# Performance work log

Measured on AMD Instinct MI355X. Metric: run time of the kernel, lower is better.

The kernel has to match this reference:

```python
import jax, jax.numpy as jnp
import numpy as np

# Dimensions
T = 1024      # tokens
D = 1024      # d_model
DFF = 1024    # expert intermediate dim
R = 64        # tucker rank (r_in == r_out)
G = 8         # n_group
E = 32        # experts_per_group
NEXP = G * E  # 256 routed experts
K = 8         # top-k


def setup_inputs() -> dict:
    key = jax.random.key(0)
    ks = jax.random.split(key, 12)
    s = 0.02
    return {
        "x": jax.random.normal(ks[0], (T, D), jnp.float32),
        "Wg": jax.random.normal(ks[1], (D, NEXP), jnp.float32) * s,
        "uin_gate": jax.random.normal(ks[2], (G, D, R), jnp.float32) * s,
        "core_gate": jax.random.normal(ks[3], (G, E, R, R), jnp.float32) * s,
        "uout_gate": jax.random.normal(ks[4], (G, R, DFF), jnp.float32) * s,
        "uin_up": jax.random.normal(ks[5], (G, D, R), jnp.float32) * s,
        "core_up": jax.random.normal(ks[6], (G, E, R, R), jnp.float32) * s,
        "uout_up": jax.random.normal(ks[7], (G, R, DFF), jnp.float32) * s,
        "uin_down": jax.random.normal(ks[8], (G, DFF, R), jnp.float32) * s,
        "core_down": jax.random.normal(ks[9], (G, E, R, R), jnp.float32) * s,
        "uout_down": jax.random.normal(ks[10], (G, R, D), jnp.float32) * s,
    }


def _moe_forward(x, Wg, uin_gate, core_gate, uout_gate,
                 uin_up, core_up, uout_up,
                 uin_down, core_down, uout_down):
    Tn, d = x.shape
    # Router: top-k over 256 experts, softmax over the k logits (fp32 as in torch)
    logits = x @ Wg                                   # [T, NEXP]
    w, sel = jax.lax.top_k(logits, K)                 # [T, K]
    w = jax.nn.softmax(w.astype(jnp.float32), axis=-1).astype(x.dtype)

    e = sel.reshape(-1)                               # [F] global expert id
    g = e // E                                        # [F] group id
    tok = jnp.repeat(jnp.arange(Tn), K)               # [F] source token id
    mask = (g[:, None] == jnp.arange(G)[None, :]).astype(x.dtype)  # [F, G]

    def gather_in(uin):
        # project tokens with every group's u_in once, then gather per pair
        pre = jnp.einsum('td,gdr->gtr', x, uin)       # [G, T, R]
        return pre[g, tok]                            # [F, R]

    def core_apply(xin, core):
        # per-pair Tucker core slice bmm: x.unsqueeze(1) @ core[rel_idx]
        slices = core.reshape(G * E, R, R)[e]         # [F, R, R] gather
        return jnp.einsum('fr,fro->fo', xin, slices)  # [F, R]

    def group_out(h, U):
        # per-pair group-specific projection: h[f] @ U[g_f]
        out = jnp.zeros((h.shape[0], U.shape[-1]), h.dtype)
        for gi in range(G):  # fixed small loop over 8 groups
            out = out + (h * mask[:, gi:gi + 1]) @ U[gi]
        return out

    gate_h = group_out(core_apply(gather_in(uin_gate), core_gate), uout_gate)  # [F, DFF]
    up_h = group_out(core_apply(gather_in(uin_up), core_up), uout_up)          # [F, DFF]
    act = jax.nn.silu(gate_h) * up_h                                           # SwiGLU
    xin_d = group_out(act, uin_down)                                           # [F, R]
    out_f = group_out(core_apply(xin_d, core_down), uout_down)                 # [F, D]
    out_f = out_f * w.reshape(-1)[:, None]
    # scatter-add expert outputs back to tokens
    return jax.ops.segment_sum(out_f, tok, num_segments=Tn)


def reference(x, Wg, uin_gate, core_gate, uout_gate,
              uin_up, core_up, uout_up,
              uin_down, core_down, uout_down):
    return _moe_forward(x, Wg, uin_gate, core_gate, uout_gate,
                        uin_up, core_up, uout_up,
                        uin_down, core_down, uout_down)
```

## Files before the change

### kernel.cpp

```cpp
#include <hip/hip_runtime.h>
#include <hip/hip_bf16.h>
#include <math.h>


#define T_ 1024
#define D_ 1024
#define DFF_ 1024
#define R_ 64
#define G_ 8
#define E_ 32
#define NEXP_ 256
#define K_ 8
#define F_ 8192
#define LKZ_ 8
#define LTB_ 8
#define PKZ_ 2
#define DKZ_ 4
#define LP_ 72

typedef short bf16x8 __attribute__((ext_vector_type(8)));
typedef float f32x4 __attribute__((ext_vector_type(4)));

__device__ __forceinline__ unsigned short f2bf(float f) {
  unsigned int u = __float_as_uint(f);
  u += 0x7fffu + ((u >> 16) & 1u);
  return (unsigned short)(u >> 16);
}

__device__ __forceinline__ void stage_tile(short* dst, const unsigned short* src,
                                           int gp, int tid) {
  for (int idx = tid; idx < 512; idx += 256) {
    int r = idx >> 3, c8 = (idx & 7) << 3;
    *(uint4*)&dst[r * LP_ + c8] = *(const uint4*)&src[(size_t)r * gp + c8];
  }
}

__device__ __forceinline__ void stage_tile_guard(short* dst, const unsigned short* src,
                                                 int gp, int rows_valid, int tid) {
  for (int idx = tid; idx < 512; idx += 256) {
    int r = idx >> 3, c8 = (idx & 7) << 3;
    uint4 v = make_uint4(0u, 0u, 0u, 0u);
    if (r < rows_valid) v = *(const uint4*)&src[(size_t)r * gp + c8];
    *(uint4*)&dst[r * LP_ + c8] = v;
  }
}

__device__ __forceinline__ void mma_strip(const short* As, const short* Bs,
                                          int ms, int lane, f32x4* acc) {
  int lm = lane & 15;
  int lk = (lane >> 4) << 3;
#pragma unroll
  for (int kc = 0; kc < 64; kc += 32) {
    bf16x8 a = *(const bf16x8*)&As[(ms + lm) * LP_ + kc + lk];
#pragma unroll
    for (int nt = 0; nt < 4; ++nt) {
      bf16x8 b = *(const bf16x8*)&Bs[(nt * 16 + lm) * LP_ + kc + lk];
      acc[nt] = __builtin_amdgcn_mfma_f32_16x16x32_bf16(a, b, acc[nt], 0, 0, 0);
    }
  }
}

__global__ __launch_bounds__(256) void k_prep_logits(
    const float* __restrict__ x, const float* __restrict__ Wg,
    const float* __restrict__ s0, const float* __restrict__ s1,
    const float* __restrict__ s2, const float* __restrict__ s3,
    const float* __restrict__ s4, const float* __restrict__ s5,
    unsigned short* __restrict__ xb,
    unsigned short* __restrict__ d0, unsigned short* __restrict__ d1,
    unsigned short* __restrict__ d2, unsigned short* __restrict__ d3,
    unsigned short* __restrict__ d4, unsigned short* __restrict__ d5,
    int* __restrict__ cnt, float* __restrict__ lp) {
  __shared__ float shbuf[64 * 65];
  int b = blockIdx.x;
  if (b < 896) {
    int id = b >> 7, rem = b & 127, g = rem >> 4, tile = rem & 15;
    if (id == 6) {
      size_t base = ((size_t)g * 16 + tile) * 8192;
      for (int i = threadIdx.x; i < 2048; i += 256) {
        size_t idx = base + (size_t)i * 4;
        float4 v = *(const float4*)&x[idx];
        xb[idx + 0] = f2bf(v.x);
        xb[idx + 1] = f2bf(v.y);
        xb[idx + 2] = f2bf(v.z);
        xb[idx + 3] = f2bf(v.w);
      }
      if (g == 0 && tile == 0) cnt[threadIdx.x] = 0;
      return;
    }
    const float* src = id == 0 ? s0 : id == 1 ? s1 : id == 2 ? s2 : id == 3 ? s3 : id == 4 ? s4 : s5;
    unsigned short* dst = id == 0 ? d0 : id == 1 ? d1 : id == 2 ? d2 : id == 3 ? d3 : id == 4 ? d4 : d5;
    if (id < 3) {
      int r0 = tile * 64;
      for (int idx = threadIdx.x; idx < 4096; idx += 256) {
        int r = idx >> 6, c = idx & 63;
        shbuf[r * 65 + c] = src[((size_t)g * 1024 + r0 + r) * 64 + c];
      }
      __syncthreads();
      for (int idx = threadIdx.x; idx < 4096; idx += 256) {
        int c = idx >> 6, r = idx & 63;
        dst[((size_t)g * 64 + c) * 1024 + r0 + r] = f2bf(shbuf[r * 65 + c]);
      }
    } else {
      int c0 = tile * 64;
      for (int idx = threadIdx.x; idx < 4096; idx += 256) {
        int r = idx >> 6, c = idx & 63;
        shbuf[r * 65 + c] = src[((size_t)g * 64 + r) * 1024 + c0 + c];
      }
      __syncthreads();
      if (id == 5) {
        for (int idx = threadIdx.x; idx < 4096; idx += 256) {
          int c = idx >> 6, r = idx & 63;
          dst[(size_t)(c0 + c) * 512 + g * 64 + r] = f2bf(shbuf[r * 65 + c]);
        }
      } else {
        for (int idx = threadIdx.x; idx < 4096; idx += 256) {
          int c = idx >> 6, r = idx & 63;
          dst[((size_t)g * 1024 + c0 + c) * 64 + r] = f2bf(shbuf[r * 65 + c]);
        }
      }
    }
    return;
  }
  int lb = b - 896;
  int t0 = (lb & 127) * LTB_;
  int z = lb >> 7;
  int e = threadIdx.x;
  float* xs = shbuf;
  float a[LTB_] = {};
  int dc = z * 128;
  {
    int idx = threadIdx.x * 4;
    int tl = idx >> 7, d = idx & 127;
    *(float4*)&xs[tl * 128 + d] = *(const float4*)&x[(size_t)(t0 + tl) * D_ + dc + d];
  }
  __syncthreads();
#pragma unroll 8
  for (int d2 = 0; d2 < 128; ++d2) {
    float wv = Wg[(size_t)(dc + d2) * NEXP_ + e];
#pragma unroll
    for (int j = 0; j < LTB_; ++j) a[j] = fmaf(xs[j * 128 + d2], wv, a[j]);
  }
  size_t base = (size_t)z * T_ * NEXP_;
#pragma unroll
  for (int j = 0; j < LTB_; ++j)
    lp[base + (size_t)(t0 + j) * NEXP_ + e] = a[j];
}

__global__ __launch_bounds__(256) void k_pre_topk(
    const unsigned short* __restrict__ xb,
    const unsigned short* __restrict__ uinT_g, const unsigned short* __restrict__ uinT_u,
    const float* __restrict__ lp,
    float* __restrict__ Pgp, float* __restrict__ Pup,
    int* __restrict__ sel, float* __restrict__ wsm,
    int* __restrict__ rank, int* __restrict__ cnt) {
  __shared__ short sh2[2 * 64 * LP_];
  int b = blockIdx.x;
  if (b < 512) {
    int tile = b & 15, g = (b >> 4) & 7, zz = b >> 7;
    int gu = zz >> 1, kz = zz & 1;
    const unsigned short* U = gu ? uinT_u : uinT_g;
    float* P = gu ? Pup : Pgp;
    int t0 = tile * 64;
    short* As = sh2;
    short* Bs = sh2 + 64 * LP_;
    int tid = threadIdx.x, lane = tid & 63, ms = (tid >> 6) * 16;
    f32x4 acc[4] = {};
    int dlo = kz * (D_ / PKZ_);
    for (int dc = dlo; dc < dlo + D_ / PKZ_; dc += 64) {
      stage_tile(As, xb + (size_t)t0 * D_ + dc, D_, tid);
      stage_tile(Bs, U + (size_t)g * 64 * 1024 + dc, 1024, tid);
      __syncthreads();
      mma_strip(As, Bs, ms, lane, acc);
      __syncthreads();
    }
    int lm = lane & 15, lq = (lane >> 4) * 4;
#pragma unroll
    for (int nt = 0; nt < 4; ++nt)
#pragma unroll
      for (int r = 0; r < 4; ++r)
        P[((size_t)(kz * G_ + g) * T_ + t0 + ms + lq + r) * R_ + nt * 16 + lm] = acc[nt][r];
    return;
  }
  int tb = b - 512;
  int wave = threadIdx.x >> 6;
  int lane = threadIdx.x & 63;
  int t = tb * 4 + wave;
  float v[4];
  int idx[4];
#pragma unroll
  for (int j = 0; j < 4; ++j) {
    idx[j] = lane + 64 * j;
    float s = 0.f;
#pragma unroll
    for (int z = 0; z < LKZ_; ++z)
      s += lp[(size_t)z * T_ * NEXP_ + (size_t)t * NEXP_ + idx[j]];
    v[j] = s;
  }
  float topv[K_];
  int topi[K_];
#pragma unroll
  for (int k = 0; k < K_; ++k) {
    float bv = v[0];
    int bi = idx[0];
#pragma unroll
    for (int j = 1; j < 4; ++j)
      if (v[j] > bv || (v[j] == bv && idx[j] < bi)) { bv = v[j]; bi = idx[j]; }
#pragma unroll
    for (int off = 32; off > 0; off >>= 1) {
      float ov = __shfl_xor(bv, off);
      int oi = __shfl_xor(bi, off);
      if (ov > bv || (ov == bv && oi < bi)) { bv = ov; bi = oi; }
    }
    topv[k] = bv;
    topi[k] = bi;
#pragma unroll
    for (int j = 0; j < 4; ++j)
      if (idx[j] == bi) v[j] = -INFINITY;
  }
  float m = topv[0];
  float ev[K_];
  float s = 0.f;
#pragma unroll
  for (int k = 0; k < K_; ++k) { ev[k] = expf(topv[k] - m); s += ev[k]; }
  float inv = 1.f / s;
  if (lane < K_) {
    sel[t * K_ + lane] = topi[lane];
    wsm[t * K_ + lane] = ev[lane] * inv;
    rank[t * K_ + lane] = atomicAdd(&cnt[topi[lane]], 1);
  }
}

__global__ __launch_bounds__(256) void k_scan(const int* __restrict__ cnt,
                                              int* __restrict__ off) {
  __shared__ int s[NEXP_];
  int i = threadIdx.x;
  s[i] = cnt[i];
  __syncthreads();
  for (int d = 1; d < NEXP_; d <<= 1) {
    int v = (i >= d) ? s[i - d] : 0;
    __syncthreads();
    s[i] += v;
    __syncthreads();
  }
  off[i + 1] = s[i];
  if (i == 0) off[0] = 0;
}

__global__ __launch_bounds__(256) void k_core_gu(const float* __restrict__ Pgp,
                                                 const float* __restrict__ Pup,
                                                 const float* __restrict__ core_g,
                                                 const float* __restrict__ core_u,
                                                 const int* __restrict__ sel,
                                                 const int* __restrict__ rank,
                                                 const int* __restrict__ off,
                                                 unsigned short* __restrict__ xgb,
                                                 unsigned short* __restrict__ xub) {
  int pl = threadIdx.x >> 6;
  int o = threadIdx.x & 63;
  int f = blockIdx.x * 4 + pl;
  int t = f >> 3;
  int e = sel[f];
  int g = e >> 5;
  int p = off[e] + rank[f];
  __shared__ float rg[4][64], ru[4][64];
  float sg = 0.f, su = 0.f;
#pragma unroll
  for (int kz = 0; kz < PKZ_; ++kz) {
    sg += Pgp[((size_t)(kz * G_ + g) * T_ + t) * R_ + o];
    su += Pup[((size_t)(kz * G_ + g) * T_ + t) * R_ + o];
  }
  rg[pl][o] = sg;
  ru[pl][o] = su;
  __syncthreads();
  const float* cg = core_g + (size_t)e * R_ * R_;
  const float* cu = core_u + (size_t)e * R_ * R_;
  float ag = 0.f, au = 0.f;
#pragma unroll 8
  for (int r = 0; r < R_; ++r) {
    ag = fmaf(rg[pl][r], cg[r * R_ + o], ag);
    au = fmaf(ru[pl][r], cu[r * R_ + o], au);
  }
  xgb[(size_t)p * R_ + o] = f2bf(ag);
  xub[(size_t)p * R_ + o] = f2bf(au);
}

__global__ __launch_bounds__(256) void k_fused_ad(const unsigned short* __restrict__ xgb,
                                                  const unsigned short* __restrict__ xub,
                                                  const unsigned short* __restrict__ uoutT_g,
                                                  const unsigned short* __restrict__ uoutT_u,
                                                  const unsigned short* __restrict__ uinT_d,
                                                  const int* __restrict__ off,
                                                  float* __restrict__ xdp) {
  int g = blockIdx.y;
  int kz = blockIdx.z;
  int p0 = off[g * E_];
  int pend = off[g * E_ + E_];
  int ntiles = (pend - p0 + 63) >> 6;
  __shared__ short Ag[64 * LP_], Au[64 * LP_];
  __shared__ short Bg[64 * LP_], Bu[64 * LP_], Bd[64 * LP_];
  __shared__ short Pt[64 * LP_];
  int tid = threadIdx.x, lane = tid & 63, ms = (tid >> 6) * 16;
  int lm = lane & 15, lq = (lane >> 4) * 4;
  for (int tile = blockIdx.x; tile < ntiles; tile += gridDim.x) {
    int pbase = p0 + tile * 64;
    int rv = pend - pbase; if (rv > 64) rv = 64;
    stage_tile_guard(Ag, xgb + (size_t)pbase * R_, R_, rv, tid);
    stage_tile_guard(Au, xub + (size_t)pbase * R_, R_, rv, tid);
    f32x4 accd[4] = {};
#pragma unroll
    for (int c4 = 0; c4 < 4; ++c4) {
      int cc = kz * (DFF_ / DKZ_) + c4 * 64;
      stage_tile(Bg, uoutT_g + ((size_t)g * DFF_ + cc) * R_, R_, tid);
      stage_tile(Bu, uoutT_u + ((size_t)g * DFF_ + cc) * R_, R_, tid);
      stage_tile(Bd, uinT_d + (size_t)g * 64 * 1024 + cc, 1024, tid);
      __syncthreads();
      f32x4 accg[4] = {}, accu[4] = {};
      mma_strip(Ag, Bg, ms, lane, accg);
      mma_strip(Au, Bu, ms, lane, accu);
#pragma unroll
      for (int nt = 0; nt < 4; ++nt)
#pragma unroll
        for (int r = 0; r < 4; ++r) {
          float gv = accg[nt][r];
          float av = gv / (1.f + expf(-gv)) * accu[nt][r];
          Pt[(ms + lq + r) * LP_ + nt * 16 + lm] = (short)f2bf(av);
        }
      mma_strip(Pt, Bd, ms, lane, accd);
      __syncthreads();
    }
#pragma unroll
    for (int nt = 0; nt < 4; ++nt)
#pragma unroll
      for (int r = 0; r < 4; ++r) {
        int p = pbase + ms + lq + r;
        if (p < pend) xdp[((size_t)kz * F_ + p) * R_ + nt * 16 + lm] = accd[nt][r];
      }
    __syncthreads();
  }
}

__global__ __launch_bounds__(256) void k_down_accY(const float* __restrict__ xdp,
                                                   const float* __restrict__ core_d,
                                                   const int* __restrict__ sel,
                                                   const int* __restrict__ rank,
                                                   const float* __restrict__ wsm,
                                                   const int* __restrict__ off,
                                                   unsigned short* __restrict__ Ybf) {
  int t = blockIdx.x;
  int w = threadIdx.x >> 6, o = threadIdx.x & 63;
  __shared__ float xs[4][64];
  __shared__ float yl[4][G_][64];
  float y[G_] = {};
#pragma unroll
  for (int kk = 0; kk < 2; ++kk) {
    int f = t * K_ + w * 2 + kk;
    int e = sel[f];
    int g = e >> 5;
    int p = off[e] + rank[f];
    float s = 0.f;
#pragma unroll
    for (int kz = 0; kz < DKZ_; ++kz) s += xdp[((size_t)kz * F_ + p) * R_ + o];
    __syncthreads();
    xs[w][o] = s;
    __syncthreads();
    const float* cd = core_d + (size_t)e * R_ * R_;
    float a = 0.f;
#pragma unroll 8
    for (int r = 0; r < R_; ++r) a = fmaf(xs[w][r], cd[r * R_ + o], a);
    y[g] += wsm[f] * a;
  }
#pragma unroll
  for (int g = 0; g < G_; ++g) yl[w][g][o] = y[g];
  __syncthreads();
  for (int idx = threadIdx.x; idx < 512; idx += 256) {
    int g = idx >> 6, oo = idx & 63;
    float v = yl[0][g][oo] + yl[1][g][oo] + yl[2][g][oo] + yl[3][g][oo];
    Ybf[(size_t)t * 512 + g * 64 + oo] = f2bf(v);
  }
}

__global__ __launch_bounds__(256) void k_fin(const unsigned short* __restrict__ Ybf,
                                             const unsigned short* __restrict__ Uod2T,
                                             float* __restrict__ out) {
  int t0 = blockIdx.x * 64;
  int d0 = blockIdx.y * 64;
  __shared__ short As[64 * LP_], Bs[64 * LP_];
  __shared__ float Os[64 * 68];
  int tid = threadIdx.x, lane = tid & 63, ms = (tid >> 6) * 16;
  int lm = lane & 15, lq = (lane >> 4) * 4;
  f32x4 acc[4] = {};
  for (int kc = 0; kc < 512; kc += 64) {
    stage_tile(As, Ybf + (size_t)t0 * 512 + kc, 512, tid);
    stage_tile(Bs, Uod2T + (size_t)d0 * 512 + kc, 512, tid);
    __syncthreads();
    mma_strip(As, Bs, ms, lane, acc);
    __syncthreads();
  }
#pragma unroll
  for (int nt = 0; nt < 4; ++nt)
#pragma unroll
    for (int r = 0; r < 4; ++r)
      Os[(ms + lq + r) * 68 + nt * 16 + lm] = acc[nt][r];
  __syncthreads();
  for (int idx = tid; idx < 1024; idx += 256) {
    int r = idx >> 4, c4 = (idx & 15) << 2;
    *(float4*)&out[(size_t)(t0 + r) * D_ + d0 + c4] = *(const float4*)&Os[r * 68 + c4];
  }
}

extern "C" void kernel_launch(void* const* d_in, const int* in_sizes, int n_in,
                              void* d_out, int out_size, void* d_ws, size_t ws_size,
                              hipStream_t stream) {
  const float* x = (const float*)d_in[0];
  const float* Wg = (const float*)d_in[1];
  const float* uin_gate = (const float*)d_in[2];
  const float* core_gate = (const float*)d_in[3];
  const float* uout_gate = (const float*)d_in[4];
  const float* uin_up = (const float*)d_in[5];
  const float* core_up = (const float*)d_in[6];
  const float* uout_up = (const float*)d_in[7];
  const float* uin_down = (const float*)d_in[8];
  const float* core_down = (const float*)d_in[9];
  const float* uout_down = (const float*)d_in[10];
  float* out = (float*)d_out;

  char* ws = (char*)d_ws;
  size_t o = 0;
  auto alloc = [&](size_t bytes) { size_t r = o; o = (o + bytes + 255) & ~(size_t)255; return r; };
  size_t o_lp = alloc((size_t)LKZ_ * T_ * NEXP_ * 4);
  size_t o_sel = alloc(F_ * 4);
  size_t o_wsm = alloc(F_ * 4);
  size_t o_rank = alloc(F_ * 4);
  size_t o_cnt = alloc(NEXP_ * 4);
  size_t o_off = alloc((NEXP_ + 1) * 4);
  size_t o_xb = alloc((size_t)T_ * D_ * 2);
  size_t o_uinT_g = alloc((size_t)G_ * 64 * 1024 * 2);
  size_t o_uinT_u = alloc((size_t)G_ * 64 * 1024 * 2);
  size_t o_uinT_d = alloc((size_t)G_ * 64 * 1024 * 2);
  size_t o_uoutT_g = alloc((size_t)G_ * 1024 * 64 * 2);
  size_t o_uoutT_u = alloc((size_t)G_ * 1024 * 64 * 2);
  size_t o_Uod2T = alloc((size_t)D_ * 512 * 2);
  size_t o_xgb = alloc((size_t)F_ * R_ * 2);
  size_t o_xub = alloc((size_t)F_ * R_ * 2);
  size_t o_Y = alloc((size_t)T_ * 512 * 2);
  size_t o_pgp = alloc((size_t)PKZ_ * G_ * T_ * R_ * 4);
  size_t o_pup = alloc((size_t)PKZ_ * G_ * T_ * R_ * 4);
  size_t o_xdp = alloc((size_t)DKZ_ * F_ * R_ * 4);
  (void)ws_size;

  float* lp = (float*)(ws + o_lp);
  int* sel = (int*)(ws + o_sel);
  float* wsm = (float*)(ws + o_wsm);
  int* rank = (int*)(ws + o_rank);
  int* cnt = (int*)(ws + o_cnt);
  int* off = (int*)(ws + o_off);
  unsigned short* xb = (unsigned short*)(ws + o_xb);
  unsigned short* uinT_g = (unsigned short*)(ws + o_uinT_g);
  unsigned short* uinT_u = (unsigned short*)(ws + o_uinT_u);
  unsigned short* uinT_d = (unsigned short*)(ws + o_uinT_d);
  unsigned short* uoutT_g = (unsigned short*)(ws + o_uoutT_g);
  unsigned short* uoutT_u = (unsigned short*)(ws + o_uoutT_u);
  unsigned short* Uod2T = (unsigned short*)(ws + o_Uod2T);
  unsigned short* xgb = (unsigned short*)(ws + o_xgb);
  unsigned short* xub = (unsigned short*)(ws + o_xub);
  unsigned short* Ybf = (unsigned short*)(ws + o_Y);
  float* pgp = (float*)(ws + o_pgp);
  float* pup = (float*)(ws + o_pup);
  float* xdp = (float*)(ws + o_xdp);

  k_prep_logits<<<1920, 256, 0, stream>>>(x, Wg, uin_gate, uin_up, uin_down,
                                          uout_gate, uout_up, uout_down, xb,
                                          uinT_g, uinT_u, uinT_d,
                                          uoutT_g, uoutT_u, Uod2T, cnt, lp);
  k_pre_topk<<<768, 256, 0, stream>>>(xb, uinT_g, uinT_u, lp, pgp, pup, sel, wsm, rank, cnt);
  k_scan<<<1, 256, 0, stream>>>(cnt, off);
  k_core_gu<<<F_ / 4, 256, 0, stream>>>(pgp, pup, core_gate, core_up, sel, rank, off, xgb, xub);
  k_fused_ad<<<dim3(16, G_, DKZ_), 256, 0, stream>>>(xgb, xub, uoutT_g, uoutT_u, uinT_d, off, xdp);
  k_down_accY<<<T_, 256, 0, stream>>>(xdp, core_down, sel, rank, wsm, off, Ybf);
  k_fin<<<dim3(16, 16), 256, 0, stream>>>(Ybf, Uod2T, out);
}
```

Before: 201.9 us.

## Fuse router logits with top-k in-block and merge scan into pre-projection kernel

The router now computes each token's full 256 logits inside one 1024-thread block, reducing the split-K partials in shared memory and doing top-k/softmax in the same block. This removes the global partial-logit buffer and its read-back. The scan is folded into the pre-projection kernel as an extra block, and the counter zeroing moves to a memset, which drops one launch. As a trade-off, the prep/transpose blocks now run with 1024 threads, so most of their threads sit idle, and each router block does more serial work.

Result: slower. 255.8 us (+26.7%).

```diff
diff --git a/kernel.cpp b/kernel.cpp
--- a/kernel.cpp
+++ b/kernel.cpp
@@ -12,8 +12,6 @@
 #define NEXP_ 256
 #define K_ 8
 #define F_ 8192
-#define LKZ_ 8
-#define LTB_ 8
 #define PKZ_ 2
 #define DKZ_ 4
 #define LP_ 72
@@ -60,7 +58,7 @@
   }
 }
 
-__global__ __launch_bounds__(256) void k_prep_logits(
+__global__ __launch_bounds__(1024) void k_prep_router(
     const float* __restrict__ x, const float* __restrict__ Wg,
     const float* __restrict__ s0, const float* __restrict__ s1,
     const float* __restrict__ s2, const float* __restrict__ s3,
@@ -69,14 +67,16 @@
     unsigned short* __restrict__ d0, unsigned short* __restrict__ d1,
     unsigned short* __restrict__ d2, unsigned short* __restrict__ d3,
     unsigned short* __restrict__ d4, unsigned short* __restrict__ d5,
-    int* __restrict__ cnt, float* __restrict__ lp) {
-  __shared__ float shbuf[64 * 65];
+    int* __restrict__ cnt, int* __restrict__ sel,
+    float* __restrict__ wsm, int* __restrict__ rank) {
+  __shared__ float shbuf[12288];
   int b = blockIdx.x;
+  int tid = threadIdx.x;
   if (b < 896) {
     int id = b >> 7, rem = b & 127, g = rem >> 4, tile = rem & 15;
     if (id == 6) {
       size_t base = ((size_t)g * 16 + tile) * 8192;
-      for (int i = threadIdx.x; i < 2048; i += 256) {
+      for (int i = tid; i < 2048; i += 1024) {
         size_t idx = base + (size_t)i * 4;
         float4 v = *(const float4*)&x[idx];
         xb[idx + 0] = f2bf(v.x);
@@ -84,36 +84,35 @@
         xb[idx + 2] = f2bf(v.z);
         xb[idx + 3] = f2bf(v.w);
       }
-      if (g == 0 && tile == 0) cnt[threadIdx.x] = 0;
       return;
     }
     const float* src = id == 0 ? s0 : id == 1 ? s1 : id == 2 ? s2 : id == 3 ? s3 : id == 4 ? s4 : s5;
     unsigned short* dst = id == 0 ? d0 : id == 1 ? d1 : id == 2 ? d2 : id == 3 ? d3 : id == 4 ? d4 : d5;
     if (id < 3) {
       int r0 = tile * 64;
-      for (int idx = threadIdx.x; idx < 4096; idx += 256) {
+      for (int idx = tid; idx < 4096; idx += 1024) {
         int r = idx >> 6, c = idx & 63;
         shbuf[r * 65 + c] = src[((size_t)g * 1024 + r0 + r) * 64 + c];
       }
       __syncthreads();
-      for (int idx = threadIdx.x; idx < 4096; idx += 256) {
+      for (int idx = tid; idx < 4096; idx += 1024) {
         int c = idx >> 6, r = idx & 63;
         dst[((size_t)g * 64 + c) * 1024 + r0 + r] = f2bf(shbuf[r * 65 + c]);
       }
     } else {
       int c0 = tile * 64;
-      for (int idx = threadIdx.x; idx < 4096; idx += 256) {
+      for (int idx = tid; idx < 4096; idx += 1024) {
         int r = idx >> 6, c = idx & 63;
         shbuf[r * 65 + c] = src[((size_t)g * 64 + r) * 1024 + c0 + c];
       }
       __syncthreads();
       if (id == 5) {
-        for (int idx = threadIdx.x; idx < 4096; idx += 256) {
+        for (int idx = tid; idx < 4096; idx += 1024) {
           int c = idx >> 6, r = idx & 63;
           dst[(size_t)(c0 + c) * 512 + g * 64 + r] = f2bf(shbuf[r * 65 + c]);
         }
       } else {
-        for (int idx = threadIdx.x; idx < 4096; idx += 256) {
+        for (int idx = tid; idx < 4096; idx += 1024) {
           int c = idx >> 6, r = idx & 63;
           dst[((size_t)g * 1024 + c0 + c) * 64 + r] = f2bf(shbuf[r * 65 + c]);
         }
@@ -121,39 +120,96 @@
     }
     return;
   }
-  int lb = b - 896;
-  int t0 = (lb & 127) * LTB_;
-  int z = lb >> 7;
-  int e = threadIdx.x;
+  int rb = b - 896;
+  int t0 = rb * 4;
+  int e = tid & 255;
+  int kc = tid >> 8;
   float* xs = shbuf;
-  float a[LTB_] = {};
-  int dc = z * 128;
   {
-    int idx = threadIdx.x * 4;
-    int tl = idx >> 7, d = idx & 127;
-    *(float4*)&xs[tl * 128 + d] = *(const float4*)&x[(size_t)(t0 + tl) * D_ + dc + d];
-  }
-  __syncthreads();
+    int tl = tid >> 8, d = (tid & 255) * 4;
+    *(float4*)&xs[tl * 1024 + d] = *(const float4*)&x[(size_t)(t0 + tl) * D_ + d];
+  }
+  __syncthreads();
+  float alo[4] = {}, ahi[4] = {};
+  int dbase = kc * 256;
 #pragma unroll 8
   for (int d2 = 0; d2 < 128; ++d2) {
-    float wv = Wg[(size_t)(dc + d2) * NEXP_ + e];
-#pragma unroll
-    for (int j = 0; j < LTB_; ++j) a[j] = fmaf(xs[j * 128 + d2], wv, a[j]);
-  }
-  size_t base = (size_t)z * T_ * NEXP_;
-#pragma unroll
-  for (int j = 0; j < LTB_; ++j)
-    lp[base + (size_t)(t0 + j) * NEXP_ + e] = a[j];
-}
-
-__global__ __launch_bounds__(256) void k_pre_topk(
+    float wv = Wg[(size_t)(dbase + d2) * NEXP_ + e];
+#pragma unroll
+    for (int j = 0; j < 4; ++j) alo[j] = fmaf(xs[j * 1024 + dbase + d2], wv, alo[j]);
+  }
+#pragma unroll 8
+  for (int d2 = 128; d2 < 256; ++d2) {
+    float wv = Wg[(size_t)(dbase + d2) * NEXP_ + e];
+#pragma unroll
+    for (int j = 0; j < 4; ++j) ahi[j] = fmaf(xs[j * 1024 + dbase + d2], wv, ahi[j]);
+  }
+  float* part = shbuf + 4096;
+#pragma unroll
+  for (int j = 0; j < 4; ++j) {
+    part[(2 * kc) * 1024 + e * 4 + j] = alo[j];
+    part[(2 * kc + 1) * 1024 + e * 4 + j] = ahi[j];
+  }
+  __syncthreads();
+  {
+    int j = tid >> 8;
+    float s = 0.f;
+#pragma unroll
+    for (int z = 0; z < 8; ++z) s += part[z * 1024 + e * 4 + j];
+    shbuf[j * 256 + e] = s;
+  }
+  __syncthreads();
+  int w = tid >> 6;
+  if (w < 4) {
+    int lane = tid & 63;
+    int t = t0 + w;
+    const float* lg = shbuf + w * 256;
+    float v[4];
+    int idx[4];
+#pragma unroll
+    for (int j = 0; j < 4; ++j) { idx[j] = lane + 64 * j; v[j] = lg[idx[j]]; }
+    float topv[K_];
+    int topi[K_];
+#pragma unroll
+    for (int k = 0; k < K_; ++k) {
+      float bv = v[0];
+      int bi = idx[0];
+#pragma unroll
+      for (int j = 1; j < 4; ++j)
+        if (v[j] > bv || (v[j] == bv && idx[j] < bi)) { bv = v[j]; bi = idx[j]; }
+#pragma unroll
+      for (int off = 32; off > 0; off >>= 1) {
+        float ov = __shfl_xor(bv, off);
+        int oi = __shfl_xor(bi, off);
+        if (ov > bv || (ov == bv && oi < bi)) { bv = ov; bi = oi; }
+      }
+      topv[k] = bv;
+      topi[k] = bi;
+#pragma unroll
+      for (int j = 0; j < 4; ++j)
+        if (idx[j] == bi) v[j] = -INFINITY;
+    }
+    float m = topv[0];
+    float ev[K_];
+    float s = 0.f;
+#pragma unroll
+    for (int k = 0; k < K_; ++k) { ev[k] = expf(topv[k] - m); s += ev[k]; }
+    float inv = 1.f / s;
+    if (lane < K_) {
+      sel[t * K_ + lane] = topi[lane];
+      wsm[t * K_ + lane] = ev[lane] * inv;
+      rank[t * K_ + lane] = atomicAdd(&cnt[topi[lane]], 1);
+    }
+  }
+}
+
+__global__ __launch_bounds__(256) void k_pre_scan(
     const unsigned short* __restrict__ xb,
     const unsigned short* __restrict__ uinT_g, const unsigned short* __restrict__ uinT_u,
-    const float* __restrict__ lp,
     float* __restrict__ Pgp, float* __restrict__ Pup,
-    int* __restrict__ sel, float* __restrict__ wsm,
-    int* __restrict__ rank, int* __restrict__ cnt) {
+    const int* __restrict__ cnt, int* __restrict__ off) {
   __shared__ short sh2[2 * 64 * LP_];
+  __shared__ int ssc[NEXP_];
   int b = blockIdx.x;
   if (b < 512) {
     int tile = b & 15, g = (b >> 4) & 7, zz = b >> 7;
@@ -181,68 +237,16 @@
         P[((size_t)(kz * G_ + g) * T_ + t0 + ms + lq + r) * R_ + nt * 16 + lm] = acc[nt][r];
     return;
   }
-  int tb = b - 512;
-  int wave = threadIdx.x >> 6;
-  int lane = threadIdx.x & 63;
-  int t = tb * 4 + wave;
-  float v[4];
-  int idx[4];
-#pragma unroll
-  for (int j = 0; j < 4; ++j) {
-    idx[j] = lane + 64 * j;
-    float s = 0.f;
-#pragma unroll
-    for (int z = 0; z < LKZ_; ++z)
-      s += lp[(size_t)z * T_ * NEXP_ + (size_t)t * NEXP_ + idx[j]];
-    v[j] = s;
-  }
-  float topv[K_];
-  int topi[K_];
-#pragma unroll
-  for (int k = 0; k < K_; ++k) {
-    float bv = v[0];
-    int bi = idx[0];
-#pragma unroll
-    for (int j = 1; j < 4; ++j)
-      if (v[j] > bv || (v[j] == bv && idx[j] < bi)) { bv = v[j]; bi = idx[j]; }
-#pragma unroll
-    for (int off = 32; off > 0; off >>= 1) {
-      float ov = __shfl_xor(bv, off);
-      int oi = __shfl_xor(bi, off);
-      if (ov > bv || (ov == bv && oi < bi)) { bv = ov; bi = oi; }
-    }
-    topv[k] = bv;
-    topi[k] = bi;
-#pragma unroll
-    for (int j = 0; j < 4; ++j)
-      if (idx[j] == bi) v[j] = -INFINITY;
-  }
-  float m = topv[0];
-  float ev[K_];
-  float s = 0.f;
-#pragma unroll
-  for (int k = 0; k < K_; ++k) { ev[k] = expf(topv[k] - m); s += ev[k]; }
-  float inv = 1.f / s;
-  if (lane < K_) {
-    sel[t * K_ + lane] = topi[lane];
-    wsm[t * K_ + lane] = ev[lane] * inv;
-    rank[t * K_ + lane] = atomicAdd(&cnt[topi[lane]], 1);
-  }
-}
-
-__global__ __launch_bounds__(256) void k_scan(const int* __restrict__ cnt,
-                                              int* __restrict__ off) {
-  __shared__ int s[NEXP_];
   int i = threadIdx.x;
-  s[i] = cnt[i];
+  ssc[i] = cnt[i];
   __syncthreads();
   for (int d = 1; d < NEXP_; d <<= 1) {
-    int v = (i >= d) ? s[i - d] : 0;
-    __syncthreads();
-    s[i] += v;
-    __syncthreads();
-  }
-  off[i + 1] = s[i];
+    int v = (i >= d) ? ssc[i - d] : 0;
+    __syncthreads();
+    ssc[i] += v;
+    __syncthreads();
+  }
+  off[i + 1] = ssc[i];
   if (i == 0) off[0] = 0;
 }
 
@@ -427,7 +431,6 @@
   char* ws = (char*)d_ws;
   size_t o = 0;
   auto alloc = [&](size_t bytes) { size_t r = o; o = (o + bytes + 255) & ~(size_t)255; return r; };
-  size_t o_lp = alloc((size_t)LKZ_ * T_ * NEXP_ * 4);
   size_t o_sel = alloc(F_ * 4);
   size_t o_wsm = alloc(F_ * 4);
   size_t o_rank = alloc(F_ * 4);
@@ -448,7 +451,6 @@
   size_t o_xdp = alloc((size_t)DKZ_ * F_ * R_ * 4);
   (void)ws_size;
 
-  float* lp = (float*)(ws + o_lp);
   int* sel = (int*)(ws + o_sel);
   float* wsm = (float*)(ws + o_wsm);
   int* rank = (int*)(ws + o_rank);
@@ -468,12 +470,14 @@
   float* pup = (float*)(ws + o_pup);
   float* xdp = (float*)(ws + o_xdp);
 
-  k_prep_logits<<<1920, 256, 0, stream>>>(x, Wg, uin_gate, uin_up, uin_down,
-                                          uout_gate, uout_up, uout_down, xb,
-                                          uinT_g, uinT_u, uinT_d,
-                                          uoutT_g, uoutT_u, Uod2T, cnt, lp);
-  k_pre_topk<<<768, 256, 0, stream>>>(xb, uinT_g, uinT_u, lp, pgp, pup, sel, wsm, rank, cnt);
-  k_scan<<<1, 256, 0, stream>>>(cnt, off);
+  hipMemsetAsync(cnt, 0, NEXP_ * 4, stream);
+
+  k_prep_router<<<1152, 1024, 0, stream>>>(x, Wg, uin_gate, uin_up, uin_down,
+                                           uout_gate, uout_up, uout_down, xb,
+                                           uinT_g, uinT_u, uinT_d,
+                                           uoutT_g, uoutT_u, Uod2T,
+                                           cnt, sel, wsm, rank);
+  k_pre_scan<<<513, 256, 0, stream>>>(xb, uinT_g, uinT_u, pgp, pup, cnt, off);
   k_core_gu<<<F_ / 4, 256, 0, stream>>>(pgp, pup, core_gate, core_up, sel, rank, off, xgb, xub);
   k_fused_ad<<<dim3(16, G_, DKZ_), 256, 0, stream>>>(xgb, xub, uoutT_g, uoutT_u, uinT_d, off, xdp);
   k_down_accY<<<T_, 256, 0, stream>>>(xdp, core_down, sel, rank, wsm, off, Ybf);
```
